# Optimization experiments

Hardware: AMD Instinct MI355X
Metric: run time of the kernel (lower is better)

Reference implementation:

```python
import jax, jax.numpy as jnp
import numpy as np

H = 512
E = 300
V = 32000
B, L, T = 32, 64, 32

def setup_inputs() -> dict:
    key = jax.random.key(0)
    ks = jax.random.split(key, 24)
    n = jax.random.normal
    inp = {
        "enc_h": n(ks[0], (B, L, 2 * H), jnp.float32),
        "prev_s": n(ks[1], (B, H), jnp.float32),
        "target_word": jax.random.randint(ks[2], (B, T), 0, V),
        # frozen embedding table
        "embed": n(ks[3], (V, E), jnp.float32) * 0.1,
        # attention: W_a (HxH), U_a (2H->H), linear (H->1)
        "W_a": n(ks[4], (H, H), jnp.float32) * 0.001,
        "b_a": jnp.zeros((H,), jnp.float32),
        "U_a": n(ks[5], (2 * H, H), jnp.float32) * 0.001,
        "b_Ua": jnp.zeros((H,), jnp.float32),
        "v_w": n(ks[6], (H,), jnp.float32) * 0.01,
        "v_b": jnp.zeros((1,), jnp.float32),
        # decoder cell, gates stacked as [z | r | s] along output dim
        "W_emb": n(ks[7], (E, 3 * H), jnp.float32) * 0.01,
        "b_emb": jnp.zeros((3 * H,), jnp.float32),
        "W_hid_zr": n(ks[8], (H, 2 * H), jnp.float32) * 0.01,
        "b_hid_zr": jnp.zeros((2 * H,), jnp.float32),
        "W_hid_s": n(ks[9], (H, H), jnp.float32) * 0.01,
        "b_hid_s": jnp.zeros((H,), jnp.float32),
        "W_ctx": n(ks[10], (2 * H, 3 * H), jnp.float32) * 0.01,
        "b_ctx": jnp.zeros((3 * H,), jnp.float32),
        # hid2word
        "W_out": n(ks[11], (H, V), jnp.float32) * 0.02,
        "b_out": jnp.zeros((V,), jnp.float32),
    }
    return inp

def _decode(enc_h, prev_s, target_word, embed, W_a, b_a, U_a, b_Ua, v_w, v_b,
            W_emb, b_emb, W_hid_zr, b_hid_zr, W_hid_s, b_hid_s, W_ctx, b_ctx,
            W_out, b_out):
    # enc_h: B x L x 2H. Precompute U_a(enc_h) once (loop-invariant).
    Uh = jnp.einsum('bld,dh->blh', enc_h, U_a) + b_Ua  # B x L x H
    target_emb = embed[target_word]                    # B x T x E (frozen)

    def step(s, emb_t):
        # Bahdanau attention
        out_s = s @ W_a + b_a                                   # B x H
        scores = jnp.tanh(out_s[:, None, :] + Uh) @ v_w + v_b   # B x L
        attn = jax.nn.softmax(scores, axis=1)                   # B x L
        ctx = jnp.einsum('bld,bl->bd', enc_h, attn)             # B x 2H
        # GRU-like cell, gates stacked [z | r | s]
        ge = emb_t @ W_emb + b_emb          # B x 3H
        gh = s @ W_hid_zr + b_hid_zr        # B x 2H (z, r)
        gc = ctx @ W_ctx + b_ctx            # B x 3H
        z = jax.nn.sigmoid(ge[:, :H] + gh[:, :H] + gc[:, :H])
        r = jax.nn.sigmoid(ge[:, H:2 * H] + gh[:, H:] + gc[:, H:2 * H])
        s_tilde = jnp.tanh(ge[:, 2 * H:] + (r * s) @ W_hid_s + b_hid_s + gc[:, 2 * H:])
        s_new = (1.0 - z) * s + z * s_tilde
        return s_new, s_new

    _, s_seq = jax.lax.scan(step, prev_s, jnp.swapaxes(target_emb, 0, 1))
    s_seq = jnp.swapaxes(s_seq, 0, 1)                # B x T x H
    return jnp.einsum('bth,hv->btv', s_seq, W_out) + b_out  # B x T x V

def reference(enc_h, prev_s, target_word, embed, W_a, b_a, U_a, b_Ua, v_w, v_b,
              W_emb, b_emb, W_hid_zr, b_hid_zr, W_hid_s, b_hid_s, W_ctx, b_ctx,
              W_out, b_out):
    return _decode(enc_h, prev_s, target_word, embed, W_a, b_a, U_a, b_Ua, v_w, v_b,
                   W_emb, b_emb, W_hid_zr, b_hid_zr, W_hid_s, b_hid_s, W_ctx, b_ctx,
                   W_out, b_out)
```

## Files before the change

### kernel.cpp

```cpp
#include <hip/hip_runtime.h>
#include <cstdint>

#define HH   512
#define HD2  1024
#define HD3  1536
#define EE   300
#define VV   32000
#define BB   32
#define LLn  64
#define TT   32

typedef unsigned short u16;
typedef __attribute__((ext_vector_type(8))) short short8;
typedef __attribute__((ext_vector_type(4))) float f32x4;

__device__ __forceinline__ float fast_tanh(float x) {
    float e = __expf(2.f * x);
    return 1.f - 2.f / (e + 1.f);
}
__device__ __forceinline__ float fast_sigmoid(float x) {
    float e = __expf(-x);
    return 1.f / (1.f + e);
}
__device__ __forceinline__ u16 f2bf(float x) {
    union { float f; unsigned u; } v; v.f = x;
    unsigned r = v.u + 0x7FFFu + ((v.u >> 16) & 1u);
    return (u16)(r >> 16);
}
__device__ __forceinline__ u16 f_hi_trunc(float x) {
    union { float f; unsigned u; } v; v.f = x;
    return (u16)(v.u >> 16);
}
__device__ __forceinline__ u16 f_lo_trunc(float x) {
    union { float f; unsigned u; } v; v.f = x;
    float res = x - __uint_as_float(v.u & 0xFFFF0000u);
    union { float f; unsigned u; } w; w.f = res;
    return (u16)(w.u >> 16);
}
__device__ __forceinline__ float bf2f(u16 x) {
    union { unsigned u; float f; } v; v.u = ((unsigned)x) << 16;
    return v.f;
}

__global__ __launch_bounds__(256) void conv_hilo(
    const float* __restrict__ src, const int* __restrict__ gather,
    int rows_out, int cols_out, int rows_valid, int cols_valid,
    u16* __restrict__ hi, u16* __restrict__ lo)
{
    int idx = blockIdx.x * 256 + threadIdx.x;
    if (idx >= rows_out * cols_out) return;
    int r = idx / cols_out, c = idx - r * cols_out;
    float x = 0.f;
    if (r < rows_valid && c < cols_valid) {
        int sr = gather ? gather[r] : r;
        x = src[(size_t)sr * cols_valid + c];
    }
    hi[idx] = f_hi_trunc(x);
    lo[idx] = f_lo_trunc(x);
}

__global__ __launch_bounds__(256) void conv_bf16(
    const float* __restrict__ src, u16* __restrict__ dst, int n)
{
    int idx = blockIdx.x * 256 + threadIdx.x;
    if (idx < n) dst[idx] = f2bf(src[idx]);
}

template<bool HILO>
__global__ __launch_bounds__(256) void transpose_conv(
    const float* __restrict__ src, int K, int N, int noff, int dld,
    u16* __restrict__ dhi, u16* __restrict__ dlo)
{
    __shared__ float t[64][65];
    const int nt = blockIdx.x, ktile = blockIdx.y, tid = threadIdx.x;
    const int n0 = nt * 64, k0 = ktile * 64;
#pragma unroll 4
    for (int i = 0; i < 16; i++) {
        int kr = i * 4 + (tid >> 6);
        int nc = tid & 63;
        t[kr][nc] = src[(size_t)(k0 + kr) * N + n0 + nc];
    }
    __syncthreads();
    const int n = tid >> 2, kc = (tid & 3) * 16;
    unsigned wh[8], wl[8];
#pragma unroll
    for (int jj = 0; jj < 8; jj++) {
        float x0 = t[kc + 2 * jj][n], x1 = t[kc + 2 * jj + 1][n];
        if (HILO) {
            wh[jj] = (unsigned)f_hi_trunc(x0) | ((unsigned)f_hi_trunc(x1) << 16);
            wl[jj] = (unsigned)f_lo_trunc(x0) | ((unsigned)f_lo_trunc(x1) << 16);
        } else {
            wh[jj] = (unsigned)f2bf(x0) | ((unsigned)f2bf(x1) << 16);
        }
    }
    u16* dh = dhi + (size_t)(noff + n0 + n) * dld + k0 + kc;
    *(uint4*)(dh)     = (uint4){wh[0], wh[1], wh[2], wh[3]};
    *(uint4*)(dh + 8) = (uint4){wh[4], wh[5], wh[6], wh[7]};
    if (HILO) {
        u16* dl = dlo + (size_t)(noff + n0 + n) * dld + k0 + kc;
        *(uint4*)(dl)     = (uint4){wl[0], wl[1], wl[2], wl[3]};
        *(uint4*)(dl + 8) = (uint4){wl[4], wl[5], wl[6], wl[7]};
    }
}

template<int KSTEPS, bool BF16OUT>
__global__ __launch_bounds__(256) void pre_mfma(
    const u16* __restrict__ Ahi, const u16* __restrict__ Alo,
    const u16* __restrict__ Whi, const u16* __restrict__ Wlo,
    const float* __restrict__ bias, void* __restrict__ Cout, int N)
{
    __shared__ u16 ah[256 * 40], al[256 * 40];
    __shared__ u16 bh[64 * 40],  bl[64 * 40];
    const int nb = blockIdx.x, mb = blockIdx.y, tid = threadIdx.x;
    const int w = tid >> 6, ln = tid & 63;
    const int quad = ln >> 4, lm = ln & 15;
    const int n0 = nb * 64;
    const int K = KSTEPS * 32;

    f32x4 acc[4][4];
#pragma unroll
    for (int r = 0; r < 4; r++)
#pragma unroll
        for (int c = 0; c < 4; c++)
            acc[r][c] = (f32x4){0.f, 0.f, 0.f, 0.f};

    for (int kt = 0; kt < KSTEPS; kt++) {
        const int k0 = kt * 32;
        {
            const uint4* sh = (const uint4*)(Ahi + (size_t)(mb * 256 + tid) * K + k0);
            const uint4* sl = (const uint4*)(Alo + (size_t)(mb * 256 + tid) * K + k0);
            uint4 h0 = sh[0], h1 = sh[1], h2 = sh[2], h3 = sh[3];
            uint4 l0 = sl[0], l1 = sl[1], l2 = sl[2], l3 = sl[3];
            uint4* dh = (uint4*)(ah + tid * 40);
            dh[0] = h0; dh[1] = h1; dh[2] = h2; dh[3] = h3;
            uint4* dl = (uint4*)(al + tid * 40);
            dl[0] = l0; dl[1] = l1; dl[2] = l2; dl[3] = l3;
        }
        {
            const int kr = tid >> 3, c8 = (tid & 7) * 8;
            union { uint4 v; u16 u[8]; } uh, ul;
            uh.v = *(const uint4*)(Whi + (size_t)(k0 + kr) * N + n0 + c8);
            ul.v = *(const uint4*)(Wlo + (size_t)(k0 + kr) * N + n0 + c8);
#pragma unroll
            for (int j = 0; j < 8; j++) {
                bh[(c8 + j) * 40 + kr] = uh.u[j];
                bl[(c8 + j) * 40 + kr] = ul.u[j];
            }
        }
        __syncthreads();
        short8 afh[4], afl[4], bfh[4], bfl[4];
#pragma unroll
        for (int r = 0; r < 4; r++) {
            afh[r] = *(const short8*)(ah + ((w * 4 + r) * 16 + lm) * 40 + quad * 8);
            afl[r] = *(const short8*)(al + ((w * 4 + r) * 16 + lm) * 40 + quad * 8);
        }
#pragma unroll
        for (int c = 0; c < 4; c++) {
            bfh[c] = *(const short8*)(bh + (c * 16 + lm) * 40 + quad * 8);
            bfl[c] = *(const short8*)(bl + (c * 16 + lm) * 40 + quad * 8);
        }
#pragma unroll
        for (int r = 0; r < 4; r++)
#pragma unroll
            for (int c = 0; c < 4; c++) {
                acc[r][c] = __builtin_amdgcn_mfma_f32_16x16x32_bf16(
                    afh[r], bfh[c], acc[r][c], 0, 0, 0);
                acc[r][c] = __builtin_amdgcn_mfma_f32_16x16x32_bf16(
                    afh[r], bfl[c], acc[r][c], 0, 0, 0);
                acc[r][c] = __builtin_amdgcn_mfma_f32_16x16x32_bf16(
                    afl[r], bfh[c], acc[r][c], 0, 0, 0);
            }
        __syncthreads();
    }
#pragma unroll
    for (int r = 0; r < 4; r++) {
        int row = mb * 256 + (w * 4 + r) * 16 + quad * 4;
#pragma unroll
        for (int c = 0; c < 4; c++) {
            int col = n0 + c * 16 + lm;
            float bo = bias[col];
#pragma unroll
            for (int q2 = 0; q2 < 4; q2++) {
                float val = acc[r][c][q2] + bo;
                if (BF16OUT)
                    ((u16*)Cout)[(size_t)(row + q2) * N + col] = f2bf(val);
                else
                    ((float*)Cout)[(size_t)(row + q2) * N + col] = val;
            }
        }
    }
}

__global__ __launch_bounds__(64) void step_a(
    const u16* __restrict__ shi, const u16* __restrict__ slo, int bstride,
    const u16* __restrict__ W1hi, const u16* __restrict__ W1lo,
    float* __restrict__ gates1)
{
    const int f = blockIdx.x;
    const int ln = threadIdx.x;
    const int quad = ln >> 4, lm = ln & 15;
    const int n0 = f * 16;

    f32x4 acc0 = (f32x4){0.f, 0.f, 0.f, 0.f};
    f32x4 acc1 = (f32x4){0.f, 0.f, 0.f, 0.f};
    const u16* wh  = W1hi + (size_t)(n0 + lm) * 512 + quad * 8;
    const u16* wl  = W1lo + (size_t)(n0 + lm) * 512 + quad * 8;
    const u16* ah0 = shi + (size_t)lm * bstride + quad * 8;
    const u16* al0 = slo + (size_t)lm * bstride + quad * 8;
    const u16* ah1 = shi + (size_t)(16 + lm) * bstride + quad * 8;
    const u16* al1 = slo + (size_t)(16 + lm) * bstride + quad * 8;

#pragma unroll
    for (int kt = 0; kt < 16; kt++) {
        const int ko = kt * 32;
        short8 bh  = *(const short8*)(wh + ko);
        short8 bl  = *(const short8*)(wl + ko);
        short8 a0h = *(const short8*)(ah0 + ko);
        short8 a0l = *(const short8*)(al0 + ko);
        short8 a1h = *(const short8*)(ah1 + ko);
        short8 a1l = *(const short8*)(al1 + ko);
        acc0 = __builtin_amdgcn_mfma_f32_16x16x32_bf16(a0h, bh, acc0, 0, 0, 0);
        acc0 = __builtin_amdgcn_mfma_f32_16x16x32_bf16(a0h, bl, acc0, 0, 0, 0);
        acc0 = __builtin_amdgcn_mfma_f32_16x16x32_bf16(a0l, bh, acc0, 0, 0, 0);
        acc1 = __builtin_amdgcn_mfma_f32_16x16x32_bf16(a1h, bh, acc1, 0, 0, 0);
        acc1 = __builtin_amdgcn_mfma_f32_16x16x32_bf16(a1h, bl, acc1, 0, 0, 0);
        acc1 = __builtin_amdgcn_mfma_f32_16x16x32_bf16(a1l, bh, acc1, 0, 0, 0);
    }
    const int col = n0 + lm;
#pragma unroll
    for (int r = 0; r < 4; r++) {
        gates1[(size_t)(quad * 4 + r) * HD3 + col]        = acc0[r];
        gates1[(size_t)(16 + quad * 4 + r) * HD3 + col]   = acc1[r];
    }
}

__global__ __launch_bounds__(256) void step_b(
    const float* __restrict__ gates1, const u16* __restrict__ Uh16,
    const u16* __restrict__ Gc16, const float* __restrict__ Ge,
    const u16* __restrict__ Whs16,
    const float* __restrict__ b_a, const float* __restrict__ v_w,
    const float* __restrict__ v_b, const float* __restrict__ b_hzr,
    const float* __restrict__ b_hs,
    const float* __restrict__ s_prev, float* __restrict__ s_next,
    u16* __restrict__ sseq_hi, u16* __restrict__ sseq_lo, int t)
{
    const int q = blockIdx.x, b = blockIdx.y, tid = threadIdx.x;
    __shared__ float outs_s[HH];
    __shared__ float vw_s[HH];
    __shared__ float red[256];
    __shared__ float attn_s[LLn];
    __shared__ float rs_s[HH];
    __shared__ float zb_s[128], pst_s[128];

    outs_s[tid]       = gates1[(size_t)b * HD3 + tid]       + b_a[tid];
    outs_s[tid + 256] = gates1[(size_t)b * HD3 + tid + 256] + b_a[tid + 256];
    vw_s[tid]       = v_w[tid];
    vw_s[tid + 256] = v_w[tid + 256];
    __syncthreads();

    {
        const int lane = tid & 63, w = tid >> 6;
        for (int lt = 0; lt < 16; lt++) {
            const int l = w * 16 + lt;
            const u16* up = Uh16 + ((size_t)(b * LLn + l)) * HH;
            float acc = 0.f;
#pragma unroll
            for (int j = 0; j < 8; j++) {
                int hh = j * 64 + lane;
                acc = fmaf(fast_tanh(outs_s[hh] + bf2f(up[hh])), vw_s[hh], acc);
            }
            for (int o = 32; o > 0; o >>= 1) acc += __shfl_xor(acc, o);
            if (lane == 0) red[l] = acc;
        }
    }
    __syncthreads();

    if (tid < 64) {
        float v = red[tid] + v_b[0];
        float m = v;
        for (int o = 32; o > 0; o >>= 1) m = fmaxf(m, __shfl_xor(m, o));
        float e = __expf(v - m);
        float s = e;
        for (int o = 32; o > 0; o >>= 1) s += __shfl_xor(s, o);
        attn_s[tid] = e / s;
    }
    __syncthreads();

    const float* ge = Ge + ((size_t)(b * TT + t)) * HD3;
    const float* sp = s_prev + b * HH;

    {
        const u16* gc = Gc16 + (size_t)b * LLn * HD3 + HH;
        float g1a = 0.f, g1b = 0.f;
#pragma unroll 4
        for (int l = 0; l < LLn; l++) {
            float a = attn_s[l];
            g1a = fmaf(a, bf2f(gc[(size_t)l * HD3 + tid]),       g1a);
            g1b = fmaf(a, bf2f(gc[(size_t)l * HD3 + tid + 256]), g1b);
        }
        float gra = b_hzr[HH + tid]       + ge[HH + tid]
                  + gates1[(size_t)b * HD3 + HD2 + tid]       + g1a;
        float grb = b_hzr[HH + tid + 256] + ge[HH + tid + 256]
                  + gates1[(size_t)b * HD3 + HD2 + tid + 256] + g1b;
        rs_s[tid]       = fast_sigmoid(gra) * sp[tid];
        rs_s[tid + 256] = fast_sigmoid(grb) * sp[tid + 256];
    }
    {
        const int c = tid & 127;
        const int hq = q * 128 + c;
        if (tid < 128) {
            const u16* gc = Gc16 + (size_t)b * LLn * HD3;
            float g0 = 0.f;
#pragma unroll 4
            for (int l = 0; l < LLn; l++)
                g0 = fmaf(attn_s[l], bf2f(gc[(size_t)l * HD3 + hq]), g0);
            zb_s[c] = fast_sigmoid(b_hzr[hq] + ge[hq]
                                   + gates1[(size_t)b * HD3 + HH + hq] + g0);
        } else {
            const u16* gc = Gc16 + (size_t)b * LLn * HD3 + HD2;
            float g2 = 0.f;
#pragma unroll 4
            for (int l = 0; l < LLn; l++)
                g2 = fmaf(attn_s[l], bf2f(gc[(size_t)l * HD3 + hq]), g2);
            pst_s[c] = ge[HD2 + hq] + g2 + b_hs[hq];
        }
    }
    __syncthreads();

    {
        const int c = tid & 127, half = tid >> 7;
        const int h0 = q * 128 + c;
        const u16* wp = Whs16 + (size_t)(half * 256) * HH + h0;
        const float* rp = rs_s + half * 256;
        float a0 = 0.f, a1 = 0.f, a2 = 0.f, a3 = 0.f;
#pragma unroll 4
        for (int k = 0; k < 256; k += 4) {
            a0 = fmaf(rp[k + 0], bf2f(wp[(size_t)(k + 0) * HH]), a0);
            a1 = fmaf(rp[k + 1], bf2f(wp[(size_t)(k + 1) * HH]), a1);
            a2 = fmaf(rp[k + 2], bf2f(wp[(size_t)(k + 2) * HH]), a2);
            a3 = fmaf(rp[k + 3], bf2f(wp[(size_t)(k + 3) * HH]), a3);
        }
        red[tid] = (a0 + a1) + (a2 + a3);
    }
    __syncthreads();

    if (tid < 128) {
        const int h0 = q * 128 + tid;
        float st = fast_tanh(pst_s[tid] + red[tid] + red[128 + tid]);
        float sv = sp[h0];
        float sn = fmaf(zb_s[tid], st - sv, sv);
        s_next[(size_t)b * HH + h0] = sn;
        size_t off = ((size_t)b * TT + t) * HH + h0;
        sseq_hi[off] = f_hi_trunc(sn);
        sseq_lo[off] = f_lo_trunc(sn);
    }
}

__global__ __launch_bounds__(256) void final_gemm(
    const u16* __restrict__ Ahi, const u16* __restrict__ Alo,
    const u16* __restrict__ Wt, const float* __restrict__ b_out,
    float* __restrict__ out)
{
    __shared__ u16 ah_lds[256 * 40];
    __shared__ u16 al_lds[256 * 40];
    __shared__ u16 b_lds[64 * 40];
    const int mb = blockIdx.x, nb = blockIdx.y, tid = threadIdx.x;
    const int w = tid >> 6, ln = tid & 63;
    const int quad = ln >> 4, lm = ln & 15;
    const int n0 = nb * 64;

    f32x4 acc[4][4];
#pragma unroll
    for (int r = 0; r < 4; r++)
#pragma unroll
        for (int c = 0; c < 4; c++)
            acc[r][c] = (f32x4){0.f, 0.f, 0.f, 0.f};

    for (int kt = 0; kt < 16; kt++) {
        const int k0 = kt * 32;
        {
            const uint4* sh = (const uint4*)(Ahi + (size_t)(mb * 256 + tid) * HH + k0);
            const uint4* sl = (const uint4*)(Alo + (size_t)(mb * 256 + tid) * HH + k0);
            uint4 h0 = sh[0], h1 = sh[1], h2 = sh[2], h3 = sh[3];
            uint4 l0 = sl[0], l1 = sl[1], l2 = sl[2], l3 = sl[3];
            uint4* dh = (uint4*)(ah_lds + tid * 40);
            dh[0] = h0; dh[1] = h1; dh[2] = h2; dh[3] = h3;
            uint4* dl = (uint4*)(al_lds + tid * 40);
            dl[0] = l0; dl[1] = l1; dl[2] = l2; dl[3] = l3;
        }
        {
            const int n = tid >> 2, part = tid & 3;
            uint4 v = *(const uint4*)(Wt + (size_t)(n0 + n) * HH + k0 + part * 8);
            *(uint4*)(b_lds + n * 40 + part * 8) = v;
        }
        __syncthreads();
        short8 afh[4], afl[4], bfr[4];
#pragma unroll
        for (int r = 0; r < 4; r++) {
            afh[r] = *(const short8*)(ah_lds + ((w * 4 + r) * 16 + lm) * 40 + quad * 8);
            afl[r] = *(const short8*)(al_lds + ((w * 4 + r) * 16 + lm) * 40 + quad * 8);
        }
#pragma unroll
        for (int c = 0; c < 4; c++)
            bfr[c] = *(const short8*)(b_lds + (c * 16 + lm) * 40 + quad * 8);
#pragma unroll
        for (int r = 0; r < 4; r++)
#pragma unroll
            for (int c = 0; c < 4; c++) {
                acc[r][c] = __builtin_amdgcn_mfma_f32_16x16x32_bf16(
                    afh[r], bfr[c], acc[r][c], 0, 0, 0);
                acc[r][c] = __builtin_amdgcn_mfma_f32_16x16x32_bf16(
                    afl[r], bfr[c], acc[r][c], 0, 0, 0);
            }
        __syncthreads();
    }
#pragma unroll
    for (int r = 0; r < 4; r++) {
        int row = mb * 256 + (w * 4 + r) * 16 + quad * 4;
#pragma unroll
        for (int c = 0; c < 4; c++) {
            int col = n0 + c * 16 + lm;
            float bo = b_out[col];
#pragma unroll
            for (int q = 0; q < 4; q++)
                out[(size_t)(row + q) * VV + col] = acc[r][c][q] + bo;
        }
    }
}

extern "C" void kernel_launch(void* const* d_in, const int* in_sizes, int n_in,
                              void* d_out, int out_size, void* d_ws, size_t ws_size,
                              hipStream_t stream)
{
    const float* enc_h  = (const float*)d_in[0];
    const float* prev_s = (const float*)d_in[1];
    const int*   tw     = (const int*)  d_in[2];
    const float* embed  = (const float*)d_in[3];
    const float* W_a    = (const float*)d_in[4];
    const float* b_a    = (const float*)d_in[5];
    const float* U_a    = (const float*)d_in[6];
    const float* b_Ua   = (const float*)d_in[7];
    const float* v_w    = (const float*)d_in[8];
    const float* v_b    = (const float*)d_in[9];
    const float* W_emb  = (const float*)d_in[10];
    const float* b_emb  = (const float*)d_in[11];
    const float* W_hzr  = (const float*)d_in[12];
    const float* b_hzr  = (const float*)d_in[13];
    const float* W_hs   = (const float*)d_in[14];
    const float* b_hs   = (const float*)d_in[15];
    const float* W_ctx  = (const float*)d_in[16];
    const float* b_ctx  = (const float*)d_in[17];
    const float* W_out  = (const float*)d_in[18];
    const float* b_out  = (const float*)d_in[19];
    float* out = (float*)d_out;

    float* ws = (float*)d_ws;
    float* Ge     = ws;  ws += 1024 * 1536;
    float* gates1 = ws;  ws += 32 * 1536;
    float* s0     = ws;  ws += 32 * 512;
    float* s1     = ws;  ws += 32 * 512;
    u16* Uh16 = (u16*)ws;  ws += (2048 * 512) / 2;
    u16* Gc16 = (u16*)ws;  ws += (2048 * 1536) / 2;
    u16* sqh  = (u16*)ws;  ws += (1024 * 512) / 2;
    u16* sql  = (u16*)ws;  ws += (1024 * 512) / 2;
    u16* p0hi = (u16*)ws;  ws += (32 * 512) / 2;
    u16* p0lo = (u16*)ws;  ws += (32 * 512) / 2;
    u16* EHhi = (u16*)ws;  ws += (2048 * 1024) / 2;
    u16* EHlo = (u16*)ws;  ws += (2048 * 1024) / 2;
    u16* UAhi = (u16*)ws;  ws += (1024 * 512) / 2;
    u16* UAlo = (u16*)ws;  ws += (1024 * 512) / 2;
    u16* WChi = (u16*)ws;  ws += (1024 * 1536) / 2;
    u16* WClo = (u16*)ws;  ws += (1024 * 1536) / 2;
    u16* WEhi = (u16*)ws;  ws += (320 * 1536) / 2;
    u16* WElo = (u16*)ws;  ws += (320 * 1536) / 2;
    u16* AGhi = (u16*)ws;  ws += (1024 * 320) / 2;
    u16* AGlo = (u16*)ws;  ws += (1024 * 320) / 2;
    u16* W1hi = (u16*)ws;  ws += (1536 * 512) / 2;
    u16* W1lo = (u16*)ws;  ws += (1536 * 512) / 2;
    u16* Wt   = (u16*)ws;  ws += (32000 * 512) / 2;
    u16* Whs16= (u16*)ws;  ws += (512 * 512) / 2;

    conv_hilo<<<dim3(64),   256, 0, stream>>>(prev_s, nullptr, 32, 512, 32, 512, p0hi, p0lo);
    conv_hilo<<<dim3(8192), 256, 0, stream>>>(enc_h, nullptr, 2048, 1024, 2048, 1024, EHhi, EHlo);
    conv_hilo<<<dim3(2048), 256, 0, stream>>>(U_a,   nullptr, 1024, 512,  1024, 512,  UAhi, UAlo);
    conv_hilo<<<dim3(6144), 256, 0, stream>>>(W_ctx, nullptr, 1024, 1536, 1024, 1536, WChi, WClo);
    conv_hilo<<<dim3(1920), 256, 0, stream>>>(W_emb, nullptr, 320,  1536, 300,  1536, WEhi, WElo);
    conv_hilo<<<dim3(1280), 256, 0, stream>>>(embed, tw,      1024, 320,  1024, 300,  AGhi, AGlo);
    conv_bf16<<<dim3(1024), 256, 0, stream>>>(W_hs, Whs16, 512 * 512);
    transpose_conv<true><<<dim3(8, 8),   256, 0, stream>>>(W_a,   512, 512,   0,   512, W1hi, W1lo);
    transpose_conv<true><<<dim3(16, 8),  256, 0, stream>>>(W_hzr, 512, 1024,  512, 512, W1hi, W1lo);
    transpose_conv<false><<<dim3(500, 8),256, 0, stream>>>(W_out, 512, 32000, 0,   512, Wt, nullptr);

    pre_mfma<32, true ><<<dim3(8, 8),  256, 0, stream>>>(EHhi, EHlo, UAhi, UAlo, b_Ua,  Uh16, 512);
    pre_mfma<32, true ><<<dim3(24, 8), 256, 0, stream>>>(EHhi, EHlo, WChi, WClo, b_ctx, Gc16, 1536);
    pre_mfma<10, false><<<dim3(24, 4), 256, 0, stream>>>(AGhi, AGlo, WEhi, WElo, b_emb, Ge,   1536);

    for (int t = 0; t < TT; t++) {
        const u16* shi; const u16* slo; int bstride;
        if (t == 0) { shi = p0hi; slo = p0lo; bstride = 512; }
        else        { shi = sqh + (size_t)(t - 1) * 512;
                      slo = sql + (size_t)(t - 1) * 512; bstride = TT * 512; }
        const float* s_in = (t == 0) ? prev_s : ((t & 1) ? s0 : s1);
        float* s_out = (t & 1) ? s1 : s0;
        step_a<<<dim3(96), 64, 0, stream>>>(shi, slo, bstride, W1hi, W1lo, gates1);
        step_b<<<dim3(4, 32), 256, 0, stream>>>(gates1, Uh16, Gc16, Ge, Whs16,
                                                b_a, v_w, v_b, b_hzr, b_hs,
                                                s_in, s_out, sqh, sql, t);
    }
    final_gemm<<<dim3(4, 500), 256, 0, stream>>>(sqh, sql, Wt, b_out, out);
}
```

Before: 1.708 ms.

## Fuse recurrent steps into one persistent kernel with grid barriers; restructure output GEMM

Replaces the 64 per-timestep launches (step_a and step_b for each of 32 steps) with a single persistent kernel of 128 blocks. Blocks synchronise through an atomic-counter grid barrier, removing launch overhead and the gaps between dependent launches. The output GEMM now loads each block's full 64-column slice of W_out into LDS once and loops over all four row blocks, reading the A hi/lo fragments straight from global memory instead of staging them in LDS. The persistent kernel relies on all 128 blocks being co-resident, otherwise the spin barrier deadlocks, and the GEMM now depends on global-load latency for A and uses a larger LDS footprint.

```diff
diff --git a/kernel.cpp b/kernel.cpp
--- a/kernel.cpp
+++ b/kernel.cpp
@@ -9,6 +9,7 @@
 #define BB   32
 #define LLn  64
 #define TT   32
+#define NBLK 128
 
 typedef unsigned short u16;
 typedef __attribute__((ext_vector_type(8))) short short8;
@@ -40,6 +41,25 @@
 __device__ __forceinline__ float bf2f(u16 x) {
     union { unsigned u; float f; } v; v.u = ((unsigned)x) << 16;
     return v.f;
+}
+
+__device__ __forceinline__ void gbar(unsigned* cnt, unsigned* gen)
+{
+    __syncthreads();
+    __threadfence();
+    if (threadIdx.x == 0) {
+        unsigned g = __hip_atomic_load(gen, __ATOMIC_RELAXED, __HIP_MEMORY_SCOPE_AGENT);
+        unsigned v = __hip_atomic_fetch_add(cnt, 1u, __ATOMIC_ACQ_REL, __HIP_MEMORY_SCOPE_AGENT);
+        if (v == NBLK - 1u) {
+            __hip_atomic_store(cnt, 0u, __ATOMIC_RELAXED, __HIP_MEMORY_SCOPE_AGENT);
+            __hip_atomic_fetch_add(gen, 1u, __ATOMIC_RELEASE, __HIP_MEMORY_SCOPE_AGENT);
+        } else {
+            while (__hip_atomic_load(gen, __ATOMIC_ACQUIRE, __HIP_MEMORY_SCOPE_AGENT) == g)
+                __builtin_amdgcn_s_sleep(2);
+        }
+    }
+    __syncthreads();
+    __threadfence();
 }
 
 __global__ __launch_bounds__(256) void conv_hilo(
@@ -191,60 +211,22 @@
     }
 }
 
-__global__ __launch_bounds__(64) void step_a(
-    const u16* __restrict__ shi, const u16* __restrict__ slo, int bstride,
+__global__ __launch_bounds__(256) void rnn_loop(
     const u16* __restrict__ W1hi, const u16* __restrict__ W1lo,
-    float* __restrict__ gates1)
-{
-    const int f = blockIdx.x;
-    const int ln = threadIdx.x;
-    const int quad = ln >> 4, lm = ln & 15;
-    const int n0 = f * 16;
-
-    f32x4 acc0 = (f32x4){0.f, 0.f, 0.f, 0.f};
-    f32x4 acc1 = (f32x4){0.f, 0.f, 0.f, 0.f};
-    const u16* wh  = W1hi + (size_t)(n0 + lm) * 512 + quad * 8;
-    const u16* wl  = W1lo + (size_t)(n0 + lm) * 512 + quad * 8;
-    const u16* ah0 = shi + (size_t)lm * bstride + quad * 8;
-    const u16* al0 = slo + (size_t)lm * bstride + quad * 8;
-    const u16* ah1 = shi + (size_t)(16 + lm) * bstride + quad * 8;
-    const u16* al1 = slo + (size_t)(16 + lm) * bstride + quad * 8;
-
-#pragma unroll
-    for (int kt = 0; kt < 16; kt++) {
-        const int ko = kt * 32;
-        short8 bh  = *(const short8*)(wh + ko);
-        short8 bl  = *(const short8*)(wl + ko);
-        short8 a0h = *(const short8*)(ah0 + ko);
-        short8 a0l = *(const short8*)(al0 + ko);
-        short8 a1h = *(const short8*)(ah1 + ko);
-        short8 a1l = *(const short8*)(al1 + ko);
-        acc0 = __builtin_amdgcn_mfma_f32_16x16x32_bf16(a0h, bh, acc0, 0, 0, 0);
-        acc0 = __builtin_amdgcn_mfma_f32_16x16x32_bf16(a0h, bl, acc0, 0, 0, 0);
-        acc0 = __builtin_amdgcn_mfma_f32_16x16x32_bf16(a0l, bh, acc0, 0, 0, 0);
-        acc1 = __builtin_amdgcn_mfma_f32_16x16x32_bf16(a1h, bh, acc1, 0, 0, 0);
-        acc1 = __builtin_amdgcn_mfma_f32_16x16x32_bf16(a1h, bl, acc1, 0, 0, 0);
-        acc1 = __builtin_amdgcn_mfma_f32_16x16x32_bf16(a1l, bh, acc1, 0, 0, 0);
-    }
-    const int col = n0 + lm;
-#pragma unroll
-    for (int r = 0; r < 4; r++) {
-        gates1[(size_t)(quad * 4 + r) * HD3 + col]        = acc0[r];
-        gates1[(size_t)(16 + quad * 4 + r) * HD3 + col]   = acc1[r];
-    }
-}
-
-__global__ __launch_bounds__(256) void step_b(
-    const float* __restrict__ gates1, const u16* __restrict__ Uh16,
-    const u16* __restrict__ Gc16, const float* __restrict__ Ge,
-    const u16* __restrict__ Whs16,
+    float* __restrict__ gates1,
+    const u16* __restrict__ Uh16, const u16* __restrict__ Gc16,
+    const float* __restrict__ Ge, const u16* __restrict__ Whs16,
     const float* __restrict__ b_a, const float* __restrict__ v_w,
     const float* __restrict__ v_b, const float* __restrict__ b_hzr,
     const float* __restrict__ b_hs,
-    const float* __restrict__ s_prev, float* __restrict__ s_next,
-    u16* __restrict__ sseq_hi, u16* __restrict__ sseq_lo, int t)
-{
-    const int q = blockIdx.x, b = blockIdx.y, tid = threadIdx.x;
+    const float* __restrict__ prev_s, float* __restrict__ s0,
+    float* __restrict__ s1,
+    u16* __restrict__ sqh, u16* __restrict__ sql,
+    const u16* __restrict__ p0hi, const u16* __restrict__ p0lo,
+    unsigned* cnt, unsigned* gen)
+{
+    const int bid = blockIdx.x, tid = threadIdx.x;
+    const int b = bid >> 2, q = bid & 3;
     __shared__ float outs_s[HH];
     __shared__ float vw_s[HH];
     __shared__ float red[256];
@@ -252,107 +234,161 @@
     __shared__ float rs_s[HH];
     __shared__ float zb_s[128], pst_s[128];
 
-    outs_s[tid]       = gates1[(size_t)b * HD3 + tid]       + b_a[tid];
-    outs_s[tid + 256] = gates1[(size_t)b * HD3 + tid + 256] + b_a[tid + 256];
     vw_s[tid]       = v_w[tid];
     vw_s[tid + 256] = v_w[tid + 256];
-    __syncthreads();
-
-    {
-        const int lane = tid & 63, w = tid >> 6;
-        for (int lt = 0; lt < 16; lt++) {
-            const int l = w * 16 + lt;
-            const u16* up = Uh16 + ((size_t)(b * LLn + l)) * HH;
-            float acc = 0.f;
-#pragma unroll
-            for (int j = 0; j < 8; j++) {
-                int hh = j * 64 + lane;
-                acc = fmaf(fast_tanh(outs_s[hh] + bf2f(up[hh])), vw_s[hh], acc);
-            }
-            for (int o = 32; o > 0; o >>= 1) acc += __shfl_xor(acc, o);
-            if (lane == 0) red[l] = acc;
-        }
-    }
-    __syncthreads();
-
-    if (tid < 64) {
-        float v = red[tid] + v_b[0];
-        float m = v;
-        for (int o = 32; o > 0; o >>= 1) m = fmaxf(m, __shfl_xor(m, o));
-        float e = __expf(v - m);
-        float s = e;
-        for (int o = 32; o > 0; o >>= 1) s += __shfl_xor(s, o);
-        attn_s[tid] = e / s;
-    }
-    __syncthreads();
-
-    const float* ge = Ge + ((size_t)(b * TT + t)) * HD3;
-    const float* sp = s_prev + b * HH;
-
-    {
-        const u16* gc = Gc16 + (size_t)b * LLn * HD3 + HH;
-        float g1a = 0.f, g1b = 0.f;
+    const float ba0 = b_a[tid], ba1 = b_a[tid + 256];
+
+    for (int t = 0; t < TT; t++) {
+        {
+            const u16* shi; const u16* slo; int bstride;
+            if (t == 0) { shi = p0hi; slo = p0lo; bstride = HH; }
+            else        { shi = sqh + (size_t)(t - 1) * HH;
+                          slo = sql + (size_t)(t - 1) * HH; bstride = TT * HH; }
+            const int gw = bid * 4 + (tid >> 6);
+            if (gw < 96) {
+                const int ln = tid & 63;
+                const int quad = ln >> 4, lm = ln & 15;
+                const int n0 = gw * 16;
+                f32x4 acc0 = (f32x4){0.f, 0.f, 0.f, 0.f};
+                f32x4 acc1 = (f32x4){0.f, 0.f, 0.f, 0.f};
+                const u16* wh  = W1hi + (size_t)(n0 + lm) * HH + quad * 8;
+                const u16* wl  = W1lo + (size_t)(n0 + lm) * HH + quad * 8;
+                const u16* ah0 = shi + (size_t)lm * bstride + quad * 8;
+                const u16* al0 = slo + (size_t)lm * bstride + quad * 8;
+                const u16* ah1 = shi + (size_t)(16 + lm) * bstride + quad * 8;
+                const u16* al1 = slo + (size_t)(16 + lm) * bstride + quad * 8;
+#pragma unroll
+                for (int kt = 0; kt < 16; kt++) {
+                    const int ko = kt * 32;
+                    short8 bh  = *(const short8*)(wh + ko);
+                    short8 bl  = *(const short8*)(wl + ko);
+                    short8 a0h = *(const short8*)(ah0 + ko);
+                    short8 a0l = *(const short8*)(al0 + ko);
+                    short8 a1h = *(const short8*)(ah1 + ko);
+                    short8 a1l = *(const short8*)(al1 + ko);
+                    acc0 = __builtin_amdgcn_mfma_f32_16x16x32_bf16(a0h, bh, acc0, 0, 0, 0);
+                    acc0 = __builtin_amdgcn_mfma_f32_16x16x32_bf16(a0h, bl, acc0, 0, 0, 0);
+                    acc0 = __builtin_amdgcn_mfma_f32_16x16x32_bf16(a0l, bh, acc0, 0, 0, 0);
+                    acc1 = __builtin_amdgcn_mfma_f32_16x16x32_bf16(a1h, bh, acc1, 0, 0, 0);
+                    acc1 = __builtin_amdgcn_mfma_f32_16x16x32_bf16(a1h, bl, acc1, 0, 0, 0);
+                    acc1 = __builtin_amdgcn_mfma_f32_16x16x32_bf16(a1l, bh, acc1, 0, 0, 0);
+                }
+                const int col = n0 + lm;
+#pragma unroll
+                for (int r = 0; r < 4; r++) {
+                    gates1[(size_t)(quad * 4 + r) * HD3 + col]      = acc0[r];
+                    gates1[(size_t)(16 + quad * 4 + r) * HD3 + col] = acc1[r];
+                }
+            }
+        }
+        gbar(cnt, gen);
+
+        {
+            const float* sp_base = (t == 0) ? prev_s : ((t & 1) ? s0 : s1);
+            float* sn_base = (t & 1) ? s1 : s0;
+
+            outs_s[tid]       = gates1[(size_t)b * HD3 + tid]       + ba0;
+            outs_s[tid + 256] = gates1[(size_t)b * HD3 + tid + 256] + ba1;
+            __syncthreads();
+
+            {
+                const int lane = tid & 63, w = tid >> 6;
+                for (int lt = 0; lt < 16; lt++) {
+                    const int l = w * 16 + lt;
+                    const u16* up = Uh16 + ((size_t)(b * LLn + l)) * HH;
+                    float acc = 0.f;
+#pragma unroll
+                    for (int j = 0; j < 8; j++) {
+                        int hh = j * 64 + lane;
+                        acc = fmaf(fast_tanh(outs_s[hh] + bf2f(up[hh])), vw_s[hh], acc);
+                    }
+                    for (int o = 32; o > 0; o >>= 1) acc += __shfl_xor(acc, o);
+                    if (lane == 0) red[l] = acc;
+                }
+            }
+            __syncthreads();
+
+            if (tid < 64) {
+                float v = red[tid] + v_b[0];
+                float m = v;
+                for (int o = 32; o > 0; o >>= 1) m = fmaxf(m, __shfl_xor(m, o));
+                float e = __expf(v - m);
+                float s = e;
+                for (int o = 32; o > 0; o >>= 1) s += __shfl_xor(s, o);
+                attn_s[tid] = e / s;
+            }
+            __syncthreads();
+
+            const float* ge = Ge + ((size_t)(b * TT + t)) * HD3;
+            const float* sp = sp_base + (size_t)b * HH;
+
+            {
+                const u16* gc = Gc16 + (size_t)b * LLn * HD3 + HH;
+                float g1a = 0.f, g1b = 0.f;
 #pragma unroll 4
-        for (int l = 0; l < LLn; l++) {
-            float a = attn_s[l];
-            g1a = fmaf(a, bf2f(gc[(size_t)l * HD3 + tid]),       g1a);
-            g1b = fmaf(a, bf2f(gc[(size_t)l * HD3 + tid + 256]), g1b);
-        }
-        float gra = b_hzr[HH + tid]       + ge[HH + tid]
-                  + gates1[(size_t)b * HD3 + HD2 + tid]       + g1a;
-        float grb = b_hzr[HH + tid + 256] + ge[HH + tid + 256]
-                  + gates1[(size_t)b * HD3 + HD2 + tid + 256] + g1b;
-        rs_s[tid]       = fast_sigmoid(gra) * sp[tid];
-        rs_s[tid + 256] = fast_sigmoid(grb) * sp[tid + 256];
-    }
-    {
-        const int c = tid & 127;
-        const int hq = q * 128 + c;
-        if (tid < 128) {
-            const u16* gc = Gc16 + (size_t)b * LLn * HD3;
-            float g0 = 0.f;
+                for (int l = 0; l < LLn; l++) {
+                    float a = attn_s[l];
+                    g1a = fmaf(a, bf2f(gc[(size_t)l * HD3 + tid]),       g1a);
+                    g1b = fmaf(a, bf2f(gc[(size_t)l * HD3 + tid + 256]), g1b);
+                }
+                float gra = b_hzr[HH + tid]       + ge[HH + tid]
+                          + gates1[(size_t)b * HD3 + HD2 + tid]       + g1a;
+                float grb = b_hzr[HH + tid + 256] + ge[HH + tid + 256]
+                          + gates1[(size_t)b * HD3 + HD2 + tid + 256] + g1b;
+                rs_s[tid]       = fast_sigmoid(gra) * sp[tid];
+                rs_s[tid + 256] = fast_sigmoid(grb) * sp[tid + 256];
+            }
+            {
+                const int c = tid & 127;
+                const int hq = q * 128 + c;
+                if (tid < 128) {
+                    const u16* gc = Gc16 + (size_t)b * LLn * HD3;
+                    float g0 = 0.f;
 #pragma unroll 4
-            for (int l = 0; l < LLn; l++)
-                g0 = fmaf(attn_s[l], bf2f(gc[(size_t)l * HD3 + hq]), g0);
-            zb_s[c] = fast_sigmoid(b_hzr[hq] + ge[hq]
-                                   + gates1[(size_t)b * HD3 + HH + hq] + g0);
-        } else {
-            const u16* gc = Gc16 + (size_t)b * LLn * HD3 + HD2;
-            float g2 = 0.f;
+                    for (int l = 0; l < LLn; l++)
+                        g0 = fmaf(attn_s[l], bf2f(gc[(size_t)l * HD3 + hq]), g0);
+                    zb_s[c] = fast_sigmoid(b_hzr[hq] + ge[hq]
+                                           + gates1[(size_t)b * HD3 + HH + hq] + g0);
+                } else {
+                    const u16* gc = Gc16 + (size_t)b * LLn * HD3 + HD2;
+                    float g2 = 0.f;
 #pragma unroll 4
-            for (int l = 0; l < LLn; l++)
-                g2 = fmaf(attn_s[l], bf2f(gc[(size_t)l * HD3 + hq]), g2);
-            pst_s[c] = ge[HD2 + hq] + g2 + b_hs[hq];
-        }
-    }
-    __syncthreads();
-
-    {
-        const int c = tid & 127, half = tid >> 7;
-        const int h0 = q * 128 + c;
-        const u16* wp = Whs16 + (size_t)(half * 256) * HH + h0;
-        const float* rp = rs_s + half * 256;
-        float a0 = 0.f, a1 = 0.f, a2 = 0.f, a3 = 0.f;
+                    for (int l = 0; l < LLn; l++)
+                        g2 = fmaf(attn_s[l], bf2f(gc[(size_t)l * HD3 + hq]), g2);
+                    pst_s[c] = ge[HD2 + hq] + g2 + b_hs[hq];
+                }
+            }
+            __syncthreads();
+
+            {
+                const int c = tid & 127, half = tid >> 7;
+                const int h0 = q * 128 + c;
+                const u16* wp = Whs16 + (size_t)(half * 256) * HH + h0;
+                const float* rp = rs_s + half * 256;
+                float a0 = 0.f, a1 = 0.f, a2 = 0.f, a3 = 0.f;
 #pragma unroll 4
-        for (int k = 0; k < 256; k += 4) {
-            a0 = fmaf(rp[k + 0], bf2f(wp[(size_t)(k + 0) * HH]), a0);
-            a1 = fmaf(rp[k + 1], bf2f(wp[(size_t)(k + 1) * HH]), a1);
-            a2 = fmaf(rp[k + 2], bf2f(wp[(size_t)(k + 2) * HH]), a2);
-            a3 = fmaf(rp[k + 3], bf2f(wp[(size_t)(k + 3) * HH]), a3);
-        }
-        red[tid] = (a0 + a1) + (a2 + a3);
-    }
-    __syncthreads();
-
-    if (tid < 128) {
-        const int h0 = q * 128 + tid;
-        float st = fast_tanh(pst_s[tid] + red[tid] + red[128 + tid]);
-        float sv = sp[h0];
-        float sn = fmaf(zb_s[tid], st - sv, sv);
-        s_next[(size_t)b * HH + h0] = sn;
-        size_t off = ((size_t)b * TT + t) * HH + h0;
-        sseq_hi[off] = f_hi_trunc(sn);
-        sseq_lo[off] = f_lo_trunc(sn);
+                for (int k = 0; k < 256; k += 4) {
+                    a0 = fmaf(rp[k + 0], bf2f(wp[(size_t)(k + 0) * HH]), a0);
+                    a1 = fmaf(rp[k + 1], bf2f(wp[(size_t)(k + 1) * HH]), a1);
+                    a2 = fmaf(rp[k + 2], bf2f(wp[(size_t)(k + 2) * HH]), a2);
+                    a3 = fmaf(rp[k + 3], bf2f(wp[(size_t)(k + 3) * HH]), a3);
+                }
+                red[tid] = (a0 + a1) + (a2 + a3);
+            }
+            __syncthreads();
+
+            if (tid < 128) {
+                const int h0 = q * 128 + tid;
+                float st = fast_tanh(pst_s[tid] + red[tid] + red[128 + tid]);
+                float sv = sp[h0];
+                float sn = fmaf(zb_s[tid], st - sv, sv);
+                sn_base[(size_t)b * HH + h0] = sn;
+                size_t off = ((size_t)b * TT + t) * HH + h0;
+                sqh[off] = f_hi_trunc(sn);
+                sql[off] = f_lo_trunc(sn);
+            }
+        }
+        gbar(cnt, gen);
     }
 }
 
@@ -361,69 +397,60 @@
     const u16* __restrict__ Wt, const float* __restrict__ b_out,
     float* __restrict__ out)
 {
-    __shared__ u16 ah_lds[256 * 40];
-    __shared__ u16 al_lds[256 * 40];
-    __shared__ u16 b_lds[64 * 40];
-    const int mb = blockIdx.x, nb = blockIdx.y, tid = threadIdx.x;
+    __shared__ u16 b_lds[64 * 520];
+    const int nb = blockIdx.x, tid = threadIdx.x;
     const int w = tid >> 6, ln = tid & 63;
     const int quad = ln >> 4, lm = ln & 15;
     const int n0 = nb * 64;
 
-    f32x4 acc[4][4];
-#pragma unroll
-    for (int r = 0; r < 4; r++)
-#pragma unroll
-        for (int c = 0; c < 4; c++)
-            acc[r][c] = (f32x4){0.f, 0.f, 0.f, 0.f};
-
-    for (int kt = 0; kt < 16; kt++) {
-        const int k0 = kt * 32;
-        {
-            const uint4* sh = (const uint4*)(Ahi + (size_t)(mb * 256 + tid) * HH + k0);
-            const uint4* sl = (const uint4*)(Alo + (size_t)(mb * 256 + tid) * HH + k0);
-            uint4 h0 = sh[0], h1 = sh[1], h2 = sh[2], h3 = sh[3];
-            uint4 l0 = sl[0], l1 = sl[1], l2 = sl[2], l3 = sl[3];
-            uint4* dh = (uint4*)(ah_lds + tid * 40);
-            dh[0] = h0; dh[1] = h1; dh[2] = h2; dh[3] = h3;
-            uint4* dl = (uint4*)(al_lds + tid * 40);
-            dl[0] = l0; dl[1] = l1; dl[2] = l2; dl[3] = l3;
-        }
-        {
-            const int n = tid >> 2, part = tid & 3;
-            uint4 v = *(const uint4*)(Wt + (size_t)(n0 + n) * HH + k0 + part * 8);
-            *(uint4*)(b_lds + n * 40 + part * 8) = v;
-        }
-        __syncthreads();
-        short8 afh[4], afl[4], bfr[4];
+    for (int i = tid; i < 4096; i += 256) {
+        int n = i >> 6, slot = i & 63;
+        uint4 v = *(const uint4*)(Wt + (size_t)(n0 + n) * HH + slot * 8);
+        *(uint4*)(b_lds + n * 520 + slot * 8) = v;
+    }
+    __syncthreads();
+
+    for (int mb = 0; mb < 4; mb++) {
+        f32x4 acc[4][4];
+#pragma unroll
+        for (int r = 0; r < 4; r++)
+#pragma unroll
+            for (int c = 0; c < 4; c++)
+                acc[r][c] = (f32x4){0.f, 0.f, 0.f, 0.f};
+
+        for (int kt = 0; kt < 16; kt++) {
+            const int k0 = kt * 32;
+            short8 afh[4], afl[4], bq[4];
+#pragma unroll
+            for (int r = 0; r < 4; r++) {
+                const size_t row = (size_t)(mb * 256 + (w * 4 + r) * 16 + lm);
+                afh[r] = *(const short8*)(Ahi + row * HH + k0 + quad * 8);
+                afl[r] = *(const short8*)(Alo + row * HH + k0 + quad * 8);
+            }
+#pragma unroll
+            for (int c = 0; c < 4; c++)
+                bq[c] = *(const short8*)(b_lds + (c * 16 + lm) * 520 + k0 + quad * 8);
+#pragma unroll
+            for (int r = 0; r < 4; r++)
+#pragma unroll
+                for (int c = 0; c < 4; c++) {
+                    acc[r][c] = __builtin_amdgcn_mfma_f32_16x16x32_bf16(
+                        afh[r], bq[c], acc[r][c], 0, 0, 0);
+                    acc[r][c] = __builtin_amdgcn_mfma_f32_16x16x32_bf16(
+                        afl[r], bq[c], acc[r][c], 0, 0, 0);
+                }
+        }
 #pragma unroll
         for (int r = 0; r < 4; r++) {
-            afh[r] = *(const short8*)(ah_lds + ((w * 4 + r) * 16 + lm) * 40 + quad * 8);
-            afl[r] = *(const short8*)(al_lds + ((w * 4 + r) * 16 + lm) * 40 + quad * 8);
-        }
-#pragma unroll
-        for (int c = 0; c < 4; c++)
-            bfr[c] = *(const short8*)(b_lds + (c * 16 + lm) * 40 + quad * 8);
-#pragma unroll
-        for (int r = 0; r < 4; r++)
+            int row = mb * 256 + (w * 4 + r) * 16 + quad * 4;
 #pragma unroll
             for (int c = 0; c < 4; c++) {
-                acc[r][c] = __builtin_amdgcn_mfma_f32_16x16x32_bf16(
-                    afh[r], bfr[c], acc[r][c], 0, 0, 0);
-                acc[r][c] = __builtin_amdgcn_mfma_f32_16x16x32_bf16(
-                    afl[r], bfr[c], acc[r][c], 0, 0, 0);
-            }
-        __syncthreads();
-    }
-#pragma unroll
-    for (int r = 0; r < 4; r++) {
-        int row = mb * 256 + (w * 4 + r) * 16 + quad * 4;
-#pragma unroll
-        for (int c = 0; c < 4; c++) {
-            int col = n0 + c * 16 + lm;
-            float bo = b_out[col];
-#pragma unroll
-            for (int q = 0; q < 4; q++)
-                out[(size_t)(row + q) * VV + col] = acc[r][c][q] + bo;
+                int col = n0 + c * 16 + lm;
+                float bo = b_out[col];
+#pragma unroll
+                for (int qq = 0; qq < 4; qq++)
+                    out[(size_t)(row + qq) * VV + col] = acc[r][c][qq] + bo;
+            }
         }
     }
 }
@@ -455,6 +482,7 @@
     float* out = (float*)d_out;
 
     float* ws = (float*)d_ws;
+    unsigned* bar = (unsigned*)ws;  ws += 64;
     float* Ge     = ws;  ws += 1024 * 1536;
     float* gates1 = ws;  ws += 32 * 1536;
     float* s0     = ws;  ws += 32 * 512;
@@ -480,6 +508,8 @@
     u16* Wt   = (u16*)ws;  ws += (32000 * 512) / 2;
     u16* Whs16= (u16*)ws;  ws += (512 * 512) / 2;
 
+    hipMemsetAsync(bar, 0, 256, stream);
+
     conv_hilo<<<dim3(64),   256, 0, stream>>>(prev_s, nullptr, 32, 512, 32, 512, p0hi, p0lo);
     conv_hilo<<<dim3(8192), 256, 0, stream>>>(enc_h, nullptr, 2048, 1024, 2048, 1024, EHhi, EHlo);
     conv_hilo<<<dim3(2048), 256, 0, stream>>>(U_a,   nullptr, 1024, 512,  1024, 512,  UAhi, UAlo);
@@ -495,17 +525,11 @@
     pre_mfma<32, true ><<<dim3(24, 8), 256, 0, stream>>>(EHhi, EHlo, WChi, WClo, b_ctx, Gc16, 1536);
     pre_mfma<10, false><<<dim3(24, 4), 256, 0, stream>>>(AGhi, AGlo, WEhi, WElo, b_emb, Ge,   1536);
 
-    for (int t = 0; t < TT; t++) {
-        const u16* shi; const u16* slo; int bstride;
-        if (t == 0) { shi = p0hi; slo = p0lo; bstride = 512; }
-        else        { shi = sqh + (size_t)(t - 1) * 512;
-                      slo = sql + (size_t)(t - 1) * 512; bstride = TT * 512; }
-        const float* s_in = (t == 0) ? prev_s : ((t & 1) ? s0 : s1);
-        float* s_out = (t & 1) ? s1 : s0;
-        step_a<<<dim3(96), 64, 0, stream>>>(shi, slo, bstride, W1hi, W1lo, gates1);
-        step_b<<<dim3(4, 32), 256, 0, stream>>>(gates1, Uh16, Gc16, Ge, Whs16,
-                                                b_a, v_w, v_b, b_hzr, b_hs,
-                                                s_in, s_out, sqh, sql, t);
-    }
-    final_gemm<<<dim3(4, 500), 256, 0, stream>>>(sqh, sql, Wt, b_out, out);
-}
+    rnn_loop<<<dim3(NBLK), 256, 0, stream>>>(
+        W1hi, W1lo, gates1, Uh16, Gc16, Ge, Whs16,
+        b_a, v_w, v_b, b_hzr, b_hs,
+        prev_s, s0, s1, sqh, sql, p0hi, p0lo,
+        &bar[0], &bar[32]);
+
+    final_gemm<<<dim3(500), 256, 0, stream>>>(sqh, sql, Wt, b_out, out);
+}
```

Result: slower. 4.018 ms (+135.3%).
